# Kernel optimization log

Measured on AMD Instinct MI355X. Metric: run time of the kernel, lower is better.

## Reference

```python
import jax, jax.numpy as jnp
import numpy as np

N = 50000
E = 800000
F_IN = 128


def _gat(h, src, dst, W, a_src, a_dst, bias, heads, out_ch, concat):
    n = h.shape[0]
    z = (h @ W.T).reshape(n, heads, out_ch)              # [N,H,C]
    alpha_s = jnp.sum(z * a_src, axis=-1)                # [N,H]
    alpha_d = jnp.sum(z * a_dst, axis=-1)                # [N,H]
    logits = jax.nn.leaky_relu(alpha_s[src] + alpha_d[dst], 0.2)  # [Etot,H]
    m = jax.ops.segment_max(logits, dst, num_segments=n)
    ex = jnp.exp(logits - m[dst])
    denom = jax.ops.segment_sum(ex, dst, num_segments=n)
    w = ex / (denom[dst] + 1e-16)                        # [Etot,H]
    agg = jax.ops.segment_sum(w[:, :, None] * z[src], dst, num_segments=n)  # [N,H,C]
    if concat:
        out = agg.reshape(n, heads * out_ch)
    else:
        out = agg.mean(axis=1)
    return out + bias


def setup_inputs() -> dict:
    key = jax.random.key(0)
    ks = jax.random.split(key, 16)
    s = lambda *sh: 1.0 / np.sqrt(sh[-1])
    inp = {
        "x": jax.random.normal(ks[0], (N, F_IN), jnp.float32),
        "edge_index": jax.random.randint(ks[1], (2, E), 0, N, jnp.int64),
        # GraphConv(no_node_features=128 -> 128, aggr='add')
        "W_rel": jax.random.normal(ks[2], (128, F_IN), jnp.float32) * s(128, F_IN),
        "b_rel": jnp.zeros((128,), jnp.float32),
        "W_root": jax.random.normal(ks[3], (128, F_IN), jnp.float32) * s(128, F_IN),
        # GATConv(128 -> 8, heads=8, concat) => 64
        "W1": jax.random.normal(ks[4], (64, 128), jnp.float32) * s(64, 128),
        "a1_src": jax.random.normal(ks[5], (8, 8), jnp.float32) * 0.35,
        "a1_dst": jax.random.normal(ks[6], (8, 8), jnp.float32) * 0.35,
        "b1": jnp.zeros((64,), jnp.float32),
        # GATConv(64 -> 64, heads=1, concat=False)
        "W2": jax.random.normal(ks[7], (64, 64), jnp.float32) * s(64, 64),
        "a2_src": jax.random.normal(ks[8], (1, 64), jnp.float32) * 0.125,
        "a2_dst": jax.random.normal(ks[9], (1, 64), jnp.float32) * 0.125,
        "b2": jnp.zeros((64,), jnp.float32),
        "Wr": jax.random.normal(ks[10], (1, 64), jnp.float32) * s(1, 64),
        "br": jnp.zeros((1,), jnp.float32),
    }
    return inp


def reference(x, edge_index, W_rel, b_rel, W_root, W1, a1_src, a1_dst, b1,
              W2, a2_src, a2_dst, b2, Wr, br):
    src, dst = edge_index[0], edge_index[1]
    # GraphConv, aggr='add': W_rel @ sum_{j in N(i)} x_j + b + W_root @ x_i
    nbr = jax.ops.segment_sum(x[src], dst, num_segments=N)
    h = nbr @ W_rel.T + b_rel + x @ W_root.T
    h = jax.nn.elu(h)
    # GATConv adds self-loops by default
    loop = jnp.arange(N, dtype=edge_index.dtype)
    src2 = jnp.concatenate([src, loop])
    dst2 = jnp.concatenate([dst, loop])
    h = _gat(h, src2, dst2, W1, a1_src, a1_dst, b1, heads=8, out_ch=8, concat=True)
    h = jax.nn.elu(h)
    h = _gat(h, src2, dst2, W2, a2_src, a2_dst, b2, heads=1, out_ch=64, concat=False)
    # final 'mean' aggregation over all nodes (single graph)
    g = jnp.mean(h, axis=0, keepdims=True)               # [1,64]
    return g @ Wr.T + br                                  # [1,1]
```

## Files before the change

kernel.cpp:

```cpp
#include <hip/hip_runtime.h>
#include <hip/hip_bf16.h>
#include <math.h>

#define N_NODES 50000
#define N_EDGES 800000
#define F_IN 128
#define NBUCK 391
#define EPB 4096
#define NBB 196
#define CAP 4096
#define APITCH 264

typedef __attribute__((ext_vector_type(8))) short bf16x8;
typedef __attribute__((ext_vector_type(4))) float f32x4;
typedef __attribute__((ext_vector_type(2))) float f32x2;
typedef unsigned long long ull;

__device__ __forceinline__ float elu_f(float x)   { return x > 0.f ? x : expm1f(x); }
__device__ __forceinline__ float lrelu_f(float x) { return x > 0.f ? x : 0.2f * x; }
__device__ __forceinline__ int   clampN(int v)    { return v < 0 ? 0 : (v >= N_NODES ? N_NODES - 1 : v); }
__device__ __forceinline__ float bits2f(unsigned int u) { union { unsigned int u; float f; } x; x.u = u; return x.f; }
__device__ __forceinline__ float bf2f(unsigned short s) { return bits2f(((unsigned int)s) << 16); }
__device__ __forceinline__ unsigned short f2bfbits(float f) {
    __hip_bfloat16 b = __float2bfloat16(f);
    return __builtin_bit_cast(unsigned short, b);
}
__device__ __forceinline__ unsigned int pack2(float lo, float hi) {
    return ((unsigned int)f2bfbits(hi) << 16) | f2bfbits(lo);
}

#define CAST_X_IDS (N_NODES * 32)
#define CAST_IDS (CAST_X_IDS + 32768 + 8192 + 4096)
#define CASTB ((CAST_IDS + 255) / 256)
__global__ __launch_bounds__(256) void k_prep(const float* __restrict__ x,
                                              const float* __restrict__ W_rel,
                                              const float* __restrict__ W_root,
                                              const float* __restrict__ W1,
                                              const float* __restrict__ W2,
                                              __hip_bfloat16* __restrict__ Abuf,
                                              unsigned int* __restrict__ x8,
                                              __hip_bfloat16* __restrict__ Wc,
                                              __hip_bfloat16* __restrict__ W1b,
                                              __hip_bfloat16* __restrict__ W2b,
                                              int* __restrict__ gcount,
                                              float* __restrict__ red,
                                              int* __restrict__ done) {
    int tid = threadIdx.x;
    if (blockIdx.x == 0) {
        red[tid] = 0.f;
        if (tid < NBUCK) gcount[tid] = 0;
        if (tid + 256 < NBUCK) gcount[tid + 256] = 0;
        if (tid == 0) done[0] = 0;
    }
    int id = blockIdx.x * 256 + tid;
    if (id < CAST_X_IDS) {
        int i = id >> 5, c4 = (id & 31) * 4;
        float4 v = *(const float4*)&x[(size_t)i * 128 + c4];
        ull p = (ull)f2bfbits(v.x) | ((ull)f2bfbits(v.y) << 16)
              | ((ull)f2bfbits(v.z) << 32) | ((ull)f2bfbits(v.w) << 48);
        *(ull*)&Abuf[(size_t)i * 128 + c4] = p;
        int t = __builtin_amdgcn_cvt_pk_fp8_f32(v.x, v.y, 0, false);
        t = __builtin_amdgcn_cvt_pk_fp8_f32(v.z, v.w, t, true);
        x8[(size_t)i * 32 + (id & 31)] = (unsigned int)t;
    } else if (id < CAST_IDS) {
        int j = id - CAST_X_IDS;
        if (j < 32768) {
            int cc = j >> 8, k = j & 255;
            float v = (k < 128) ? W_rel[cc * 128 + k] : W_root[cc * 128 + (k - 128)];
            Wc[j] = __float2bfloat16(v);
        } else if (j < 32768 + 8192) {
            W1b[j - 32768] = __float2bfloat16(W1[j - 32768]);
        } else {
            W2b[j - 32768 - 8192] = __float2bfloat16(W2[j - 32768 - 8192]);
        }
    }
}

__global__ __launch_bounds__(256) void k_bscatter(const int* __restrict__ src,
                                                  const int* __restrict__ dst,
                                                  int* __restrict__ gcount,
                                                  unsigned int* __restrict__ ebuf) {
    __shared__ int hist[NBUCK];
    __shared__ int hbase[NBUCK];
    int tid = threadIdx.x;
    for (int j = tid; j < NBUCK; j += 256) hist[j] = 0;
    __syncthreads();
    int base = blockIdx.x * EPB;
    unsigned int myP[EPB / 256]; int myB[EPB / 256], myR[EPB / 256];
    #pragma unroll
    for (int t = 0; t < EPB / 256; ++t) {
        int e = base + t * 256 + tid;
        if (e < N_EDGES) {
            int d = clampN(dst[e]);
            int s = clampN(src[e]);
            myP[t] = ((unsigned int)s << 7) | (unsigned int)(d & 127);
            myB[t] = d >> 7;
            myR[t] = atomicAdd(&hist[d >> 7], 1);
        } else myB[t] = -1;
    }
    __syncthreads();
    for (int j = tid; j < NBUCK; j += 256)
        if (hist[j]) hbase[j] = j * CAP + atomicAdd(&gcount[j], hist[j]);
    __syncthreads();
    #pragma unroll
    for (int t = 0; t < EPB / 256; ++t) {
        if (myB[t] >= 0) ebuf[hbase[myB[t]] + myR[t]] = myP[t];
    }
}

__global__ __launch_bounds__(256) void k_bfinal(const unsigned int* __restrict__ ebuf,
                                                const int* __restrict__ gcount,
                                                int2* __restrict__ offs,
                                                int* __restrict__ csr) {
    __shared__ int cnt[128];
    __shared__ int cur[128];
    __shared__ int ws[4];
    int b = blockIdx.x;
    int tid = threadIdx.x;
    int node0 = b << 7;
    int k0 = b * CAP, k1 = k0 + gcount[b];
    if (tid < 128) cnt[tid] = 0;
    __syncthreads();
    for (int k = k0 + tid; k < k1; k += 256)
        atomicAdd(&cnt[ebuf[k] & 127u], 1);
    __syncthreads();
    int lane = tid & 63;
    int v = (tid < 128) ? cnt[tid] : 0;
    int x = v;
    #pragma unroll
    for (int d = 1; d < 64; d <<= 1) {
        int t = __shfl_up(x, d, 64);
        if (lane >= d) x += t;
    }
    if (lane == 63) ws[tid >> 6] = x;
    __syncthreads();
    if (tid < 128) {
        int add = (tid >> 6) ? ws[0] : 0;
        int excl = k0 + add + x - v;
        cur[tid] = excl;
        int node = node0 + tid;
        if (node < N_NODES) offs[node] = make_int2(excl, excl + v);
    }
    __syncthreads();
    for (int k = k0 + tid; k < k1; k += 256) {
        unsigned int e = ebuf[k];
        int r = atomicAdd(&cur[e & 127u], 1);
        csr[r] = (int)(e >> 7);
    }
}

__global__ __launch_bounds__(256) void k_gemm12(const unsigned int* __restrict__ x8,
                                                const int2* __restrict__ offs,
                                                const int* __restrict__ csr,
                                                const __hip_bfloat16* __restrict__ Ax,
                                                const __hip_bfloat16* __restrict__ Wc,
                                                const float* __restrict__ bias,
                                                const __hip_bfloat16* __restrict__ W1b,
                                                const float* __restrict__ a_src,
                                                const float* __restrict__ a_dst,
                                                float* __restrict__ as_o,
                                                float* __restrict__ ad_o,
                                                unsigned int* __restrict__ z8) {
    __shared__ __align__(16) short smem[64 * APITCH + 128 * 40];
    short* sAF = smem;
    short (*sW)[40] = (short(*)[40])(smem + 64 * APITCH);
    int tid = threadIdx.x;
    int lane = tid & 63, wave = tid >> 6;
    int quad = lane >> 4, l16 = lane & 15;
    int node0 = blockIdx.x * 64;

    {
        int l = tid & 31;
        for (int r8 = 0; r8 < 8; ++r8) {
            int rloc = r8 * 8 + (tid >> 5);
            int i = node0 + rloc;
            bool valid = i < N_NODES;
            int2 oe = valid ? offs[i] : make_int2(0, 0);
            int k0 = oe.x, k1 = oe.y;
            float a0 = 0.f, a1 = 0.f, a2 = 0.f, a3 = 0.f;
            for (int kb = k0; kb < k1; kb += 8) {
                int s[8]; int vm[8];
                #pragma unroll
                for (int j = 0; j < 8; ++j) {
                    int kk = kb + j;
                    vm[j] = kk < k1;
                    s[j] = csr[vm[j] ? kk : k1 - 1];
                }
                unsigned int u[8];
                #pragma unroll
                for (int j = 0; j < 8; ++j) u[j] = x8[(size_t)s[j] * 32 + l];
                #pragma unroll
                for (int j = 0; j < 8; ++j) {
                    if (vm[j]) {
                        f32x2 lo = __builtin_amdgcn_cvt_pk_f32_fp8(u[j], false);
                        f32x2 hi = __builtin_amdgcn_cvt_pk_f32_fp8(u[j], true);
                        a0 += lo.x; a1 += lo.y; a2 += hi.x; a3 += hi.y;
                    }
                }
            }
            *(ull*)&sAF[rloc * APITCH + 4 * l] = (ull)pack2(a0, a1) | ((ull)pack2(a2, a3) << 32);
        }
    }
    {
        int row = tid >> 2, c32 = (tid & 3) * 32;
        int gx = node0 + row; if (gx >= N_NODES) gx = N_NODES - 1;
        const short* xp = (const short*)Ax + (size_t)gx * 128 + c32;
        #pragma unroll
        for (int q = 0; q < 4; ++q)
            *(bf16x8*)&sAF[row * APITCH + 128 + c32 + q * 8] = *(const bf16x8*)(xp + q * 8);
    }
    __syncthreads();

    int srow = tid >> 2, schk = (tid & 3) * 8;
    const short* Wp = (const short*)Wc;
    f32x4 acc[8];
    #pragma unroll
    for (int t = 0; t < 8; ++t) acc[t] = (f32x4){0.f, 0.f, 0.f, 0.f};
    for (int k0 = 0; k0 < 256; k0 += 32) {
        #pragma unroll
        for (int it = 0; it < 2; ++it) {
            int wrow = srow + it * 64;
            *(bf16x8*)&sW[wrow][schk] = *(const bf16x8*)(Wp + (size_t)wrow * 256 + k0 + schk);
        }
        __syncthreads();
        bf16x8 a = *(const bf16x8*)&sAF[(wave * 16 + l16) * APITCH + k0 + quad * 8];
        #pragma unroll
        for (int nt = 0; nt < 8; ++nt) {
            bf16x8 b = *(const bf16x8*)&sW[nt * 16 + l16][quad * 8];
            acc[nt] = __builtin_amdgcn_mfma_f32_16x16x32_bf16(a, b, acc[nt], 0, 0, 0);
        }
        __syncthreads();
    }
    #pragma unroll
    for (int nt = 0; nt < 8; ++nt) {
        int col = nt * 16 + l16;
        float bv = bias[col];
        #pragma unroll
        for (int r = 0; r < 4; ++r) {
            int row = wave * 16 + quad * 4 + r;
            sAF[row * APITCH + col] = (short)f2bfbits(elu_f(acc[nt][r] + bv));
        }
    }
    __syncthreads();
    f32x4 acc2[4];
    #pragma unroll
    for (int t = 0; t < 4; ++t) acc2[t] = (f32x4){0.f, 0.f, 0.f, 0.f};
    const short* W1p = (const short*)W1b;
    #pragma unroll
    for (int k0 = 0; k0 < 128; k0 += 32) {
        bf16x8 a = *(const bf16x8*)&sAF[(wave * 16 + l16) * APITCH + k0 + quad * 8];
        #pragma unroll
        for (int nt = 0; nt < 4; ++nt) {
            bf16x8 b = *(const bf16x8*)(W1p + (size_t)(nt * 16 + l16) * 128 + k0 + quad * 8);
            acc2[nt] = __builtin_amdgcn_mfma_f32_16x16x32_bf16(a, b, acc2[nt], 0, 0, 0);
        }
    }
    __syncthreads();
    #pragma unroll
    for (int nt = 0; nt < 4; ++nt) {
        int col = nt * 16 + l16;
        #pragma unroll
        for (int r = 0; r < 4; ++r) {
            int row = wave * 16 + quad * 4 + r;
            smem[row * 72 + col] = (short)f2bfbits(acc2[nt][r]);
        }
    }
    __syncthreads();
    int row = tid >> 2, chunk = tid & 3;
    int gi = node0 + row;
    float v[16];
    bf16x8 c0 = *(const bf16x8*)&smem[row * 72 + chunk * 16];
    bf16x8 c1 = *(const bf16x8*)&smem[row * 72 + chunk * 16 + 8];
    #pragma unroll
    for (int j = 0; j < 8; ++j) {
        v[j]     = bf2f((unsigned short)c0[j]);
        v[8 + j] = bf2f((unsigned short)c1[j]);
    }
    float ps0 = 0.f, pd0 = 0.f, ps1 = 0.f, pd1 = 0.f;
    #pragma unroll
    for (int j = 0; j < 8; ++j) {
        ps0 += v[j] * a_src[chunk * 16 + j];
        pd0 += v[j] * a_dst[chunk * 16 + j];
        ps1 += v[8 + j] * a_src[chunk * 16 + 8 + j];
        pd1 += v[8 + j] * a_dst[chunk * 16 + 8 + j];
    }
    if (gi < N_NODES) {
        as_o[(size_t)gi * 8 + 2 * chunk]     = ps0;
        as_o[(size_t)gi * 8 + 2 * chunk + 1] = ps1;
        ad_o[(size_t)gi * 8 + 2 * chunk]     = pd0;
        ad_o[(size_t)gi * 8 + 2 * chunk + 1] = pd1;
        #pragma unroll
        for (int wi = 0; wi < 4; ++wi) {
            int t = __builtin_amdgcn_cvt_pk_fp8_f32(v[4 * wi], v[4 * wi + 1], 0, false);
            t = __builtin_amdgcn_cvt_pk_fp8_f32(v[4 * wi + 2], v[4 * wi + 3], t, true);
            z8[(size_t)gi * 16 + chunk * 4 + wi] = (unsigned int)t;
        }
    }
}

__global__ __launch_bounds__(256) void k_gat1z2(const unsigned int* __restrict__ z8,
                                                const float* __restrict__ as1,
                                                const float* __restrict__ ad1,
                                                const float* __restrict__ b1,
                                                const int2* __restrict__ offs,
                                                const int* __restrict__ csr,
                                                const __hip_bfloat16* __restrict__ W2b,
                                                const float* __restrict__ a2s,
                                                const float* __restrict__ a2d,
                                                const float* __restrict__ Wr,
                                                float* __restrict__ as2,
                                                float* __restrict__ ad2,
                                                float* __restrict__ zr) {
    __shared__ __align__(16) short sH2[16 * 72];
    __shared__ __align__(16) short sZ2[16 * 72];
    int iloc = threadIdx.x >> 4;
    int i = blockIdx.x * 16 + iloc;
    int l = threadIdx.x & 15;
    int hd = l >> 1;
    int wh = l & 7, slot = l >> 3;
    int2 oe = offs[i];
    int k0 = oe.x, k1 = oe.y;
    float ad_h = ad1[(size_t)i * 8 + hd];
    float adw  = ad1[(size_t)i * 8 + wh];
    float e_self = __expf(lrelu_f(as1[(size_t)i * 8 + hd] + ad_h));
    unsigned int uz = z8[(size_t)i * 16 + l];
    f32x2 zlo = __builtin_amdgcn_cvt_pk_f32_fp8(uz, false);
    f32x2 zhi = __builtin_amdgcn_cvt_pk_f32_fp8(uz, true);
    float acc0 = e_self * zlo.x, acc1 = e_self * zlo.y;
    float acc2 = e_self * zhi.x, acc3 = e_self * zhi.y;
    float denp = 0.f;
    for (int kb = k0; kb < k1; kb += 8) {
        int sr[4]; float er[4];
        #pragma unroll
        for (int m = 0; m < 4; ++m) {
            int kk = kb + 2 * m + slot;
            bool v = kk < k1;
            int s = csr[v ? kk : k1 - 1];
            sr[m] = s;
            er[m] = v ? __expf(lrelu_f(as1[(size_t)s * 8 + wh] + adw)) : 0.f;
            denp += er[m];
        }
        int sj[8]; float ej[8]; unsigned int u[8];
        #pragma unroll
        for (int m = 0; m < 4; ++m) {
            #pragma unroll
            for (int sb = 0; sb < 2; ++sb) {
                sj[2 * m + sb] = __shfl(sr[m], sb * 8 + hd, 16);
                ej[2 * m + sb] = __shfl(er[m], sb * 8 + hd, 16);
            }
        }
        #pragma unroll
        for (int j = 0; j < 8; ++j) u[j] = z8[(size_t)sj[j] * 16 + l];
        #pragma unroll
        for (int j = 0; j < 8; ++j) {
            f32x2 alo = __builtin_amdgcn_cvt_pk_f32_fp8(u[j], false);
            f32x2 ahi = __builtin_amdgcn_cvt_pk_f32_fp8(u[j], true);
            acc0 += ej[j] * alo.x; acc1 += ej[j] * alo.y;
            acc2 += ej[j] * ahi.x; acc3 += ej[j] * ahi.y;
        }
    }
    denp += __shfl_xor(denp, 8, 16);
    float den = __shfl(denp, hd, 16) + e_self;
    float inv = 1.f / den;
    float r0 = elu_f(acc0 * inv + b1[4 * l + 0]);
    float r1 = elu_f(acc1 * inv + b1[4 * l + 1]);
    float r2 = elu_f(acc2 * inv + b1[4 * l + 2]);
    float r3 = elu_f(acc3 * inv + b1[4 * l + 3]);
    *(ull*)&sH2[iloc * 72 + 4 * l] = (ull)pack2(r0, r1) | ((ull)pack2(r2, r3) << 32);
    __syncthreads();
    int lane = threadIdx.x & 63, wave = threadIdx.x >> 6;
    int quad = lane >> 4, l16 = lane & 15;
    f32x4 accz = (f32x4){0.f, 0.f, 0.f, 0.f};
    const short* W2p = (const short*)W2b;
    #pragma unroll
    for (int kk0 = 0; kk0 < 64; kk0 += 32) {
        bf16x8 a = *(const bf16x8*)&sH2[l16 * 72 + kk0 + quad * 8];
        bf16x8 b = *(const bf16x8*)(W2p + (size_t)(wave * 16 + l16) * 64 + kk0 + quad * 8);
        accz = __builtin_amdgcn_mfma_f32_16x16x32_bf16(a, b, accz, 0, 0, 0);
    }
    #pragma unroll
    for (int r = 0; r < 4; ++r)
        sZ2[(quad * 4 + r) * 72 + wave * 16 + l16] = (short)f2bfbits(accz[r]);
    __syncthreads();
    ull pz = *(const ull*)&sZ2[iloc * 72 + 4 * l];
    float v0 = bf2f((unsigned short)(pz & 0xffff));
    float v1 = bf2f((unsigned short)((pz >> 16) & 0xffff));
    float v2 = bf2f((unsigned short)((pz >> 32) & 0xffff));
    float v3 = bf2f((unsigned short)(pz >> 48));
    float ps = v0 * a2s[4 * l + 0] + v1 * a2s[4 * l + 1] + v2 * a2s[4 * l + 2] + v3 * a2s[4 * l + 3];
    float pd = v0 * a2d[4 * l + 0] + v1 * a2d[4 * l + 1] + v2 * a2d[4 * l + 2] + v3 * a2d[4 * l + 3];
    float pr = v0 * Wr[4 * l + 0]  + v1 * Wr[4 * l + 1]  + v2 * Wr[4 * l + 2]  + v3 * Wr[4 * l + 3];
    #pragma unroll
    for (int d = 8; d >= 1; d >>= 1) {
        ps += __shfl_xor(ps, d, 16);
        pd += __shfl_xor(pd, d, 16);
        pr += __shfl_xor(pr, d, 16);
    }
    if (l == 0) { as2[i] = ps; ad2[i] = pd; zr[i] = pr; }
}

__global__ __launch_bounds__(256) void k_gat2s(const float* __restrict__ zr,
                                               const float* __restrict__ as2,
                                               const float* __restrict__ ad2,
                                               const int2* __restrict__ offs,
                                               const int* __restrict__ csr,
                                               const float* __restrict__ b2,
                                               const float* __restrict__ Wr,
                                               const float* __restrict__ br,
                                               float* __restrict__ red,
                                               int* __restrict__ done,
                                               float* __restrict__ out) {
    __shared__ float wsum[4];
    __shared__ int lastFlag;
    int tid = threadIdx.x;
    int n = blockIdx.x * 64 + (tid >> 2);
    int r = tid & 3;
    float c = 0.f;
    if (n < N_NODES) {
        int2 oe = offs[n];
        float ad = ad2[n];
        float den = 0.f, num = 0.f;
        for (int k = oe.x + r; k < oe.y; k += 4) {
            int s = csr[k];
            float e = __expf(lrelu_f(as2[s] + ad));
            den += e;
            num += e * zr[s];
        }
        den += __shfl_xor(den, 1, 64); den += __shfl_xor(den, 2, 64);
        num += __shfl_xor(num, 1, 64); num += __shfl_xor(num, 2, 64);
        if (r == 0) {
            float es = __expf(lrelu_f(as2[n] + ad));
            den += es;
            num += es * zr[n];
            c = num / den;
        }
    }
    #pragma unroll
    for (int d = 4; d <= 32; d <<= 1) c += __shfl_xor(c, d, 64);
    int lane = tid & 63, wave = tid >> 6;
    if (lane == 0) wsum[wave] = c;
    __syncthreads();
    if (tid == 0) {
        float s = wsum[0] + wsum[1] + wsum[2] + wsum[3];
        atomicAdd(&red[blockIdx.x & 255], s);
        __threadfence();
        int old = atomicAdd(done, 1);
        lastFlag = (old == (int)gridDim.x - 1);
    }
    __syncthreads();
    if (lastFlag) {
        __threadfence();
        if (tid < 64) {
            float rv = atomicAdd(&red[tid], 0.f) + atomicAdd(&red[tid + 64], 0.f)
                     + atomicAdd(&red[tid + 128], 0.f) + atomicAdd(&red[tid + 192], 0.f);
            float p = rv * (1.0f / N_NODES) + b2[tid] * Wr[tid];
            #pragma unroll
            for (int d = 32; d >= 1; d >>= 1) p += __shfl_xor(p, d, 64);
            if (tid == 0) out[0] = p + br[0];
        }
    }
}

extern "C" void kernel_launch(void* const* d_in, const int* in_sizes, int n_in,
                              void* d_out, int out_size, void* d_ws, size_t ws_size,
                              hipStream_t stream) {
    const float* x      = (const float*)d_in[0];
    const int*   edges  = (const int*)d_in[1];
    const float* W_rel  = (const float*)d_in[2];
    const float* b_rel  = (const float*)d_in[3];
    const float* W_root = (const float*)d_in[4];
    const float* W1     = (const float*)d_in[5];
    const float* a1s    = (const float*)d_in[6];
    const float* a1d    = (const float*)d_in[7];
    const float* b1     = (const float*)d_in[8];
    const float* W2     = (const float*)d_in[9];
    const float* a2s    = (const float*)d_in[10];
    const float* a2d    = (const float*)d_in[11];
    const float* b2     = (const float*)d_in[12];
    const float* Wr     = (const float*)d_in[13];
    const float* br     = (const float*)d_in[14];
    float* out = (float*)d_out;

    const int* src = edges;
    const int* dst = edges + N_EDGES;

    char* ws = (char*)d_ws;
    size_t p = 0;
    auto alloc = [&](size_t bytes) -> void* {
        void* r = ws + p;
        p = (p + bytes + 255) & ~(size_t)255;
        return r;
    };
    unsigned int* ebuf = (unsigned int*)alloc((size_t)NBUCK * CAP * 4);
    int2*  offs    = (int2*)alloc((size_t)N_NODES * 8);
    int*   csr     = (int*)alloc((size_t)NBUCK * CAP * 4);
    int*   gcount  = (int*)alloc((size_t)NBUCK * 4);
    __hip_bfloat16* Abuf = (__hip_bfloat16*)alloc((size_t)N_NODES * 128 * 2);
    unsigned int* x8 = (unsigned int*)alloc((size_t)N_NODES * 32 * 4);
    __hip_bfloat16* Wc   = (__hip_bfloat16*)alloc((size_t)128 * 256 * 2);
    __hip_bfloat16* W1b  = (__hip_bfloat16*)alloc((size_t)64 * 128 * 2);
    __hip_bfloat16* W2b  = (__hip_bfloat16*)alloc((size_t)64 * 64 * 2);
    float* as1 = (float*)alloc((size_t)N_NODES * 8 * 4);
    float* ad1 = (float*)alloc((size_t)N_NODES * 8 * 4);
    float* as2 = (float*)alloc((size_t)N_NODES * 4);
    float* ad2 = (float*)alloc((size_t)N_NODES * 4);
    float* zr  = (float*)alloc((size_t)N_NODES * 4);
    unsigned int* z1e8 = (unsigned int*)alloc((size_t)N_NODES * 16 * 4);
    float* red = (float*)alloc(256 * 4);
    int*   done = (int*)alloc(4);

    const int MB   = (N_NODES + 63) / 64;
    const int NB16 = N_NODES / 16;

    k_prep    <<<CASTB, 256, 0, stream>>>(x, W_rel, W_root, W1, W2,
                                          Abuf, x8, Wc, W1b, W2b, gcount, red, done);
    k_bscatter<<<NBB, 256, 0, stream>>>(src, dst, gcount, ebuf);
    k_bfinal  <<<NBUCK, 256, 0, stream>>>(ebuf, gcount, offs, csr);
    k_gemm12  <<<MB, 256, 0, stream>>>(x8, offs, csr, Abuf, Wc, b_rel, W1b,
                                       a1s, a1d, as1, ad1, z1e8);
    k_gat1z2  <<<NB16, 256, 0, stream>>>(z1e8, as1, ad1, b1, offs, csr,
                                         W2b, a2s, a2d, Wr, as2, ad2, zr);
    k_gat2s   <<<MB, 256, 0, stream>>>(zr, as2, ad2, offs, csr, b2, Wr, br,
                                       red, done, out);
}
```

Before: 259.3 us.

## Split neighbor gather out of fused GEMM kernel into separate high-parallelism kernel

The CSR neighbor-sum gather moves out of k_gemm12 into a new k_gather kernel that runs 8 nodes per block over 6250 blocks. Its results go to a widened 256-column bf16 A buffer, and the x cast now writes into the second half of that buffer. The GEMM kernel then streams A tiles from global memory with much smaller shared memory, which should raise occupancy. In exchange it adds an extra launch and a round trip of about 25MB of A through global memory.

```diff
diff --git a/kernel.cpp b/kernel.cpp
--- a/kernel.cpp
+++ b/kernel.cpp
@@ -9,7 +9,6 @@
 #define EPB 4096
 #define NBB 196
 #define CAP 4096
-#define APITCH 264
 
 typedef __attribute__((ext_vector_type(8))) short bf16x8;
 typedef __attribute__((ext_vector_type(4))) float f32x4;
@@ -58,7 +57,7 @@
         float4 v = *(const float4*)&x[(size_t)i * 128 + c4];
         ull p = (ull)f2bfbits(v.x) | ((ull)f2bfbits(v.y) << 16)
               | ((ull)f2bfbits(v.z) << 32) | ((ull)f2bfbits(v.w) << 48);
-        *(ull*)&Abuf[(size_t)i * 128 + c4] = p;
+        *(ull*)&Abuf[(size_t)i * 256 + 128 + c4] = p;
         int t = __builtin_amdgcn_cvt_pk_fp8_f32(v.x, v.y, 0, false);
         t = __builtin_amdgcn_cvt_pk_fp8_f32(v.z, v.w, t, true);
         x8[(size_t)i * 32 + (id & 31)] = (unsigned int)t;
@@ -149,10 +148,39 @@
     }
 }
 
-__global__ __launch_bounds__(256) void k_gemm12(const unsigned int* __restrict__ x8,
+__global__ __launch_bounds__(256) void k_gather(const unsigned int* __restrict__ x8,
                                                 const int2* __restrict__ offs,
                                                 const int* __restrict__ csr,
-                                                const __hip_bfloat16* __restrict__ Ax,
+                                                ull* __restrict__ outNbr) {
+    int i = blockIdx.x * 8 + (threadIdx.x >> 5);
+    int l = threadIdx.x & 31;
+    int2 oe = offs[i];
+    int k0 = oe.x, k1 = oe.y;
+    float a0 = 0.f, a1 = 0.f, a2 = 0.f, a3 = 0.f;
+    for (int kb = k0; kb < k1; kb += 8) {
+        int s[8]; int vm[8];
+        #pragma unroll
+        for (int j = 0; j < 8; ++j) {
+            int kk = kb + j;
+            vm[j] = kk < k1;
+            s[j] = csr[vm[j] ? kk : k1 - 1];
+        }
+        unsigned int u[8];
+        #pragma unroll
+        for (int j = 0; j < 8; ++j) u[j] = x8[(size_t)s[j] * 32 + l];
+        #pragma unroll
+        for (int j = 0; j < 8; ++j) {
+            if (vm[j]) {
+                f32x2 lo = __builtin_amdgcn_cvt_pk_f32_fp8(u[j], false);
+                f32x2 hi = __builtin_amdgcn_cvt_pk_f32_fp8(u[j], true);
+                a0 += lo.x; a1 += lo.y; a2 += hi.x; a3 += hi.y;
+            }
+        }
+    }
+    outNbr[(size_t)i * 64 + l] = (ull)pack2(a0, a1) | ((ull)pack2(a2, a3) << 32);
+}
+
+__global__ __launch_bounds__(256) void k_gemm12(const __hip_bfloat16* __restrict__ A,
                                                 const __hip_bfloat16* __restrict__ Wc,
                                                 const float* __restrict__ bias,
                                                 const __hip_bfloat16* __restrict__ W1b,
@@ -161,69 +189,29 @@
                                                 float* __restrict__ as_o,
                                                 float* __restrict__ ad_o,
                                                 unsigned int* __restrict__ z8) {
-    __shared__ __align__(16) short smem[64 * APITCH + 128 * 40];
-    short* sAF = smem;
-    short (*sW)[40] = (short(*)[40])(smem + 64 * APITCH);
+    __shared__ __align__(16) short smem[64 * 136];
+    short (*sA)[40] = (short(*)[40])smem;
+    short (*sW)[40] = (short(*)[40])(smem + 64 * 40);
     int tid = threadIdx.x;
     int lane = tid & 63, wave = tid >> 6;
     int quad = lane >> 4, l16 = lane & 15;
     int node0 = blockIdx.x * 64;
-
-    {
-        int l = tid & 31;
-        for (int r8 = 0; r8 < 8; ++r8) {
-            int rloc = r8 * 8 + (tid >> 5);
-            int i = node0 + rloc;
-            bool valid = i < N_NODES;
-            int2 oe = valid ? offs[i] : make_int2(0, 0);
-            int k0 = oe.x, k1 = oe.y;
-            float a0 = 0.f, a1 = 0.f, a2 = 0.f, a3 = 0.f;
-            for (int kb = k0; kb < k1; kb += 8) {
-                int s[8]; int vm[8];
-                #pragma unroll
-                for (int j = 0; j < 8; ++j) {
-                    int kk = kb + j;
-                    vm[j] = kk < k1;
-                    s[j] = csr[vm[j] ? kk : k1 - 1];
-                }
-                unsigned int u[8];
-                #pragma unroll
-                for (int j = 0; j < 8; ++j) u[j] = x8[(size_t)s[j] * 32 + l];
-                #pragma unroll
-                for (int j = 0; j < 8; ++j) {
-                    if (vm[j]) {
-                        f32x2 lo = __builtin_amdgcn_cvt_pk_f32_fp8(u[j], false);
-                        f32x2 hi = __builtin_amdgcn_cvt_pk_f32_fp8(u[j], true);
-                        a0 += lo.x; a1 += lo.y; a2 += hi.x; a3 += hi.y;
-                    }
-                }
-            }
-            *(ull*)&sAF[rloc * APITCH + 4 * l] = (ull)pack2(a0, a1) | ((ull)pack2(a2, a3) << 32);
-        }
-    }
-    {
-        int row = tid >> 2, c32 = (tid & 3) * 32;
-        int gx = node0 + row; if (gx >= N_NODES) gx = N_NODES - 1;
-        const short* xp = (const short*)Ax + (size_t)gx * 128 + c32;
-        #pragma unroll
-        for (int q = 0; q < 4; ++q)
-            *(bf16x8*)&sAF[row * APITCH + 128 + c32 + q * 8] = *(const bf16x8*)(xp + q * 8);
-    }
-    __syncthreads();
-
     int srow = tid >> 2, schk = (tid & 3) * 8;
+    int ga = node0 + srow; if (ga >= N_NODES) ga = N_NODES - 1;
+    const short* Ap = (const short*)A + (size_t)ga * 256 + schk;
     const short* Wp = (const short*)Wc;
     f32x4 acc[8];
     #pragma unroll
     for (int t = 0; t < 8; ++t) acc[t] = (f32x4){0.f, 0.f, 0.f, 0.f};
     for (int k0 = 0; k0 < 256; k0 += 32) {
+        *(bf16x8*)&sA[srow][schk] = *(const bf16x8*)(Ap + k0);
         #pragma unroll
         for (int it = 0; it < 2; ++it) {
             int wrow = srow + it * 64;
             *(bf16x8*)&sW[wrow][schk] = *(const bf16x8*)(Wp + (size_t)wrow * 256 + k0 + schk);
         }
         __syncthreads();
-        bf16x8 a = *(const bf16x8*)&sAF[(wave * 16 + l16) * APITCH + k0 + quad * 8];
+        bf16x8 a = *(const bf16x8*)&sA[wave * 16 + l16][quad * 8];
         #pragma unroll
         for (int nt = 0; nt < 8; ++nt) {
             bf16x8 b = *(const bf16x8*)&sW[nt * 16 + l16][quad * 8];
@@ -238,7 +226,7 @@
         #pragma unroll
         for (int r = 0; r < 4; ++r) {
             int row = wave * 16 + quad * 4 + r;
-            sAF[row * APITCH + col] = (short)f2bfbits(elu_f(acc[nt][r] + bv));
+            smem[row * 136 + col] = (short)f2bfbits(elu_f(acc[nt][r] + bv));
         }
     }
     __syncthreads();
@@ -248,7 +236,7 @@
     const short* W1p = (const short*)W1b;
     #pragma unroll
     for (int k0 = 0; k0 < 128; k0 += 32) {
-        bf16x8 a = *(const bf16x8*)&sAF[(wave * 16 + l16) * APITCH + k0 + quad * 8];
+        bf16x8 a = *(const bf16x8*)&smem[(wave * 16 + l16) * 136 + k0 + quad * 8];
         #pragma unroll
         for (int nt = 0; nt < 4; ++nt) {
             bf16x8 b = *(const bf16x8*)(W1p + (size_t)(nt * 16 + l16) * 128 + k0 + quad * 8);
@@ -495,7 +483,7 @@
     int2*  offs    = (int2*)alloc((size_t)N_NODES * 8);
     int*   csr     = (int*)alloc((size_t)NBUCK * CAP * 4);
     int*   gcount  = (int*)alloc((size_t)NBUCK * 4);
-    __hip_bfloat16* Abuf = (__hip_bfloat16*)alloc((size_t)N_NODES * 128 * 2);
+    __hip_bfloat16* Abuf = (__hip_bfloat16*)alloc((size_t)N_NODES * 256 * 2);
     unsigned int* x8 = (unsigned int*)alloc((size_t)N_NODES * 32 * 4);
     __hip_bfloat16* Wc   = (__hip_bfloat16*)alloc((size_t)128 * 256 * 2);
     __hip_bfloat16* W1b  = (__hip_bfloat16*)alloc((size_t)64 * 128 * 2);
@@ -510,14 +498,15 @@
     int*   done = (int*)alloc(4);
 
     const int MB   = (N_NODES + 63) / 64;
+    const int NB8  = N_NODES / 8;
     const int NB16 = N_NODES / 16;
 
     k_prep    <<<CASTB, 256, 0, stream>>>(x, W_rel, W_root, W1, W2,
                                           Abuf, x8, Wc, W1b, W2b, gcount, red, done);
     k_bscatter<<<NBB, 256, 0, stream>>>(src, dst, gcount, ebuf);
     k_bfinal  <<<NBUCK, 256, 0, stream>>>(ebuf, gcount, offs, csr);
-    k_gemm12  <<<MB, 256, 0, stream>>>(x8, offs, csr, Abuf, Wc, b_rel, W1b,
-                                       a1s, a1d, as1, ad1, z1e8);
+    k_gather  <<<NB8, 256, 0, stream>>>(x8, offs, csr, (ull*)Abuf);
+    k_gemm12  <<<MB, 256, 0, stream>>>(Abuf, Wc, b_rel, W1b, a1s, a1d, as1, ad1, z1e8);
     k_gat1z2  <<<NB16, 256, 0, stream>>>(z1e8, as1, ad1, b1, offs, csr,
                                          W2b, a2s, a2d, Wr, as2, ad2, zr);
     k_gat2s   <<<MB, 256, 0, stream>>>(zr, as2, ad2, offs, csr, b2, Wr, br,
```

After: 223.2 us. 13.9% less time.
